# Performance work log

Measured on AMD Instinct MI355X. Metric: run time of the kernel, lower is better.

The kernel has to match this reference:

```python
import jax, jax.numpy as jnp
import numpy as np

N_NODES = 100000
N_EDGES = 1600000
IN_DIM, HID_DIM, OUT_DIM = 128, 128, 64


def _sage_conv(x, src, dst, W_l, W_r, b, num_nodes):
    # messages: gather source-node features, mean-aggregate at destination
    msgs = x[src]                                            # [E, D]
    agg = jax.ops.segment_sum(msgs, dst, num_segments=num_nodes)   # [N, D]
    deg = jax.ops.segment_sum(jnp.ones((src.shape[0],), x.dtype), dst,
                              num_segments=num_nodes)        # [N]
    mean = jnp.where(deg[:, None] > 0, agg / jnp.maximum(deg, 1.0)[:, None], 0.0)
    # PyG SAGEConv: lin_l(aggr) + lin_r(root); bias lives in lin_l
    return mean @ W_l + b + x @ W_r


def setup_inputs() -> dict:
    key = jax.random.key(0)
    ks = jax.random.split(key, 8)
    x = jax.random.normal(ks[0], (N_NODES, IN_DIM), dtype=jnp.float32)
    edge_index = jax.random.randint(ks[1], (2, N_EDGES), 0, N_NODES, dtype=jnp.int64)
    s1 = 1.0 / np.sqrt(IN_DIM)
    s2 = 1.0 / np.sqrt(HID_DIM)
    return {
        "x": x,
        "edge_index": edge_index,
        "W1_l": jax.random.normal(ks[2], (IN_DIM, HID_DIM), jnp.float32) * s1,
        "W1_r": jax.random.normal(ks[3], (IN_DIM, HID_DIM), jnp.float32) * s1,
        "b1": jnp.zeros((HID_DIM,), jnp.float32),
        "W2_l": jax.random.normal(ks[4], (HID_DIM, OUT_DIM), jnp.float32) * s2,
        "W2_r": jax.random.normal(ks[5], (HID_DIM, OUT_DIM), jnp.float32) * s2,
        "b2": jnp.zeros((OUT_DIM,), jnp.float32),
    }


def reference(x, edge_index, W1_l, W1_r, b1, W2_l, W2_r, b2):
    src, dst = edge_index[0], edge_index[1]  # source_to_target flow
    h = _sage_conv(x, src, dst, W1_l, W1_r, b1, N_NODES)
    h = jax.nn.relu(h)
    # dropout is identity in eval mode
    h = _sage_conv(h, src, dst, W2_l, W2_r, b2, N_NODES)
    return h
```

## Files before the change

### kernel.cpp

```cpp
#include <hip/hip_runtime.h>

#define N_NODES 100000
#define N_EDGES 1600000
#define IN_DIM 128
#define HID_DIM 128
#define OUT_DIM 64

#define BKT_SHIFT 8
#define NPB 256
#define NBKT ((N_NODES + NPB - 1) / NPB)
#define BKT_CAP 5120
#define BIN_CHUNK 4096

#define CC_CSR NBKT
#define CC_CONV (N_NODES / 4)
#define CC_WT 192

typedef __attribute__((ext_vector_type(8))) short short8;
typedef __attribute__((ext_vector_type(4))) float f32x4;
typedef __attribute__((ext_vector_type(2))) short s16x2;

__device__ __forceinline__ float bf2f(unsigned short h) {
    unsigned int u = ((unsigned int)h) << 16;
    return __builtin_bit_cast(float, u);
}
__device__ __forceinline__ unsigned short f2bf(float f) {
    unsigned int u = __builtin_bit_cast(unsigned int, f);
    u += 0x7FFFu + ((u >> 16) & 1u);
    return (unsigned short)(u >> 16);
}

#define XSCALE 21.166666f
#define XINV   0.047244094f
#define ZQ     10.583333f
#define ZINV   0.094488189f

__device__ __forceinline__ void acc_i8x4(unsigned v, s16x2& L, s16x2& H) {
    s16x2 sv = __builtin_bit_cast(s16x2, v);
    H += sv >> 8;
    L += (s16x2)(sv << 8) >> 8;
}

__device__ __forceinline__ int wswz(int m, int k, int KW) {
    return (m * KW + k) ^ ((m & 7) << 3);
}

__global__ __launch_bounds__(256) void bin_kernel(
        const int* __restrict__ src, const int* __restrict__ dst,
        int* __restrict__ cursor, unsigned* __restrict__ binned) {
    __shared__ int cnt[NBKT];
    __shared__ int sbase[NBKT];
    const int b = blockIdx.x, t = threadIdx.x;
    for (int i = t; i < NBKT; i += 256) cnt[i] = 0;
    __syncthreads();
    const int e0 = b * BIN_CHUNK;
    unsigned val[16];
    int bkt[16], rank[16];
    #pragma unroll
    for (int k = 0; k < 16; ++k) {
        int e = e0 + k * 256 + t;
        if (e < N_EDGES) {
            int d = dst[e];
            bkt[k] = d >> BKT_SHIFT;
            val[k] = (unsigned)src[e] | ((unsigned)(d & (NPB - 1)) << 17);
            rank[k] = atomicAdd(&cnt[bkt[k]], 1);
        } else {
            bkt[k] = -1;
        }
    }
    __syncthreads();
    for (int i = t; i < NBKT; i += 256)
        sbase[i] = cnt[i] ? atomicAdd(&cursor[i], cnt[i]) : 0;
    __syncthreads();
    #pragma unroll
    for (int k = 0; k < 16; ++k)
        if (bkt[k] >= 0)
            binned[(size_t)bkt[k] * BKT_CAP + sbase[bkt[k]] + rank[k]] = val[k];
}

__global__ __launch_bounds__(256) void csr_conv_kernel(
        const unsigned* __restrict__ binned, const int* __restrict__ cursor,
        int* __restrict__ offsets, int* __restrict__ csr_src,
        const float* __restrict__ x, unsigned short* __restrict__ xh,
        unsigned char* __restrict__ xq,
        const float* __restrict__ W1l, const float* __restrict__ W1r,
        const float* __restrict__ W2l, const float* __restrict__ W2r,
        unsigned short* __restrict__ WT1, unsigned short* __restrict__ WT2T) {
    int b = blockIdx.x;
    const int t = threadIdx.x;

    if (b < CC_CSR) {
        __shared__ int deg[NPB];
        __shared__ int cur[NPB];
        __shared__ int wsums[4];
        __shared__ int sbase_sh;
        const int lane = t & 63, wid = t >> 6;

        int ps = 0;
        for (int i = t; i < b; i += 256) ps += cursor[i];
        #pragma unroll
        for (int off = 32; off; off >>= 1) ps += __shfl_down(ps, off, 64);
        if (lane == 0) wsums[wid] = ps;
        deg[t] = 0;
        __syncthreads();
        if (t == 0) sbase_sh = wsums[0] + wsums[1] + wsums[2] + wsums[3];
        __syncthreads();
        const int base = sbase_sh;
        const int n0 = b << BKT_SHIFT;
        const int cnt = cursor[b];
        const unsigned* __restrict__ ebase = binned + (size_t)b * BKT_CAP;

        for (int i = t; i < cnt; i += 256)
            atomicAdd(&deg[ebase[i] >> 17], 1);
        __syncthreads();

        int d = deg[t];
        int s = d;
        #pragma unroll
        for (int off = 1; off < 64; off <<= 1) {
            int u = __shfl_up(s, off, 64);
            if (lane >= off) s += u;
        }
        if (lane == 63) wsums[wid] = s;
        __syncthreads();
        int add = 0;
        for (int w = 0; w < wid; ++w) add += wsums[w];
        const int excl = s + add - d;
        cur[t] = excl;
        const int n = n0 + t;
        if (n <= N_NODES) offsets[n] = base + excl;
        __syncthreads();

        for (int i = t; i < cnt; i += 256) {
            unsigned v = ebase[i];
            int pos = atomicAdd(&cur[v >> 17], 1);
            csr_src[base + pos] = (int)(v & 0x1FFFFu);
        }
        return;
    }

    b -= CC_CSR;
    if (b < CC_CONV) {
        const int w = t >> 6, lane = t & 63;
        const int row = b * 4 + w;
        float2 v = *(const float2*)(x + (size_t)row * 128 + lane * 2);
        unsigned pk = (unsigned)f2bf(v.x) | ((unsigned)f2bf(v.y) << 16);
        *(unsigned*)(xh + (size_t)row * 128 + lane * 2) = pk;
        int q0 = (int)__float2int_rn(fminf(fmaxf(v.x * XSCALE, -127.f), 127.f));
        int q1 = (int)__float2int_rn(fminf(fmaxf(v.y * XSCALE, -127.f), 127.f));
        *(unsigned short*)(xq + (size_t)row * 128 + lane * 2) =
            (unsigned short)((q0 & 0xFF) | ((q1 & 0xFF) << 8));
        return;
    }

    int i = (b - CC_CONV) * 256 + t;
    if (i < 128 * 256) {
        int m = i >> 8, k = i & 255;
        float v = (k < 128) ? W1l[(size_t)k * 128 + m] : W1r[(size_t)(k - 128) * 128 + m];
        WT1[wswz(m, k, 256)] = f2bf(v);
        return;
    }
    i -= 128 * 256;
    if (i < 128 * 128) {
        int j = i >> 7, k = i & 127;
        float v = (j < 64) ? W2l[(size_t)k * 64 + j] : W2r[(size_t)k * 64 + (j - 64)];
        WT2T[wswz(j, k, 128)] = f2bf(v);
    }
}

__global__ __launch_bounds__(256) void agg1_int8(
        const unsigned char* __restrict__ xq, const int* __restrict__ offsets,
        const int* __restrict__ csr_src, unsigned short* __restrict__ mh) {
    const int wv = threadIdx.x >> 6;
    const int lane = threadIdx.x & 63;
    const int slot = lane >> 3, dp = lane & 7;
    const int node = (blockIdx.x * 4 + wv) * 8 + slot;
    const int beg = offsets[node];
    const int deg = offsets[node + 1] - beg;

    s16x2 aL[4], aH[4];
    #pragma unroll
    for (int i = 0; i < 4; ++i) { aL[i] = (s16x2)0; aH[i] = (s16x2)0; }

    for (int c = 0; c < deg; c += 8) {
        int my = beg + c + dp;
        int idx8 = csr_src[my < beg + deg ? my : beg];
        #pragma unroll
        for (int jj = 0; jj < 8; ++jj) {
            if (c + jj < deg) {
                int s = __shfl(idx8, slot * 8 + jj, 64);
                uint4 v = *(const uint4*)(xq + (size_t)s * 128 + dp * 16);
                acc_i8x4(v.x, aL[0], aH[0]);
                acc_i8x4(v.y, aL[1], aH[1]);
                acc_i8x4(v.z, aL[2], aH[2]);
                acc_i8x4(v.w, aL[3], aH[3]);
            }
        }
    }

    const float inv = (deg > 0) ? XINV / (float)deg : 0.0f;
    unsigned w[8];
    #pragma unroll
    for (int d = 0; d < 4; ++d) {
        w[2 * d]     = (unsigned)f2bf((float)aL[d].x * inv)
                     | ((unsigned)f2bf((float)aH[d].x * inv) << 16);
        w[2 * d + 1] = (unsigned)f2bf((float)aL[d].y * inv)
                     | ((unsigned)f2bf((float)aH[d].y * inv) << 16);
    }
    uint4* o = (uint4*)(mh + (size_t)node * 128 + dp * 16);
    o[0] = make_uint4(w[0], w[1], w[2], w[3]);
    o[1] = make_uint4(w[4], w[5], w[6], w[7]);
}

__global__ __launch_bounds__(256) void gemm1_kernel(
        const unsigned short* __restrict__ mh, const unsigned short* __restrict__ xh,
        const unsigned short* __restrict__ WT1, const float* __restrict__ b1,
        unsigned short* __restrict__ hh) {
    __shared__ unsigned short Ws[128 * 256];
    const int t = threadIdx.x;
    {
        const uint4* s = (const uint4*)WT1;
        uint4* d = (uint4*)Ws;
        #pragma unroll
        for (int r = 0; r < 16; ++r) d[t + r * 256] = s[t + r * 256];
    }
    const int wave = t >> 6;
    const int lane = t & 63;
    const int rowbase = blockIdx.x * 128 + wave * 32;
    const int lrow = lane & 15;
    const int kq = (lane >> 4) * 8;
    const int rsw = (lrow & 7) << 3;

    f32x4 acc[2][8];
    #pragma unroll
    for (int rt = 0; rt < 2; ++rt)
        #pragma unroll
        for (int ct = 0; ct < 8; ++ct) acc[rt][ct] = (f32x4)0.f;

    int r0 = rowbase + lrow;      if (r0 > N_NODES - 1) r0 = N_NODES - 1;
    int r1 = rowbase + 16 + lrow; if (r1 > N_NODES - 1) r1 = N_NODES - 1;

    __syncthreads();

    #pragma unroll
    for (int half = 0; half < 2; ++half) {
        const unsigned short* __restrict__ A = half ? xh : mh;
        #pragma unroll
        for (int kc = 0; kc < 4; ++kc) {
            const int kofs = kc * 32 + kq;
            short8 a0 = *(const short8*)(A + (size_t)r0 * 128 + kofs);
            short8 a1 = *(const short8*)(A + (size_t)r1 * 128 + kofs);
            #pragma unroll
            for (int ct = 0; ct < 8; ++ct) {
                short8 bb = *(const short8*)&Ws[(((ct * 16 + lrow) << 8)
                                                 + (half << 7) + kofs) ^ rsw];
                acc[0][ct] = __builtin_amdgcn_mfma_f32_16x16x32_bf16(a0, bb, acc[0][ct], 0, 0, 0);
                acc[1][ct] = __builtin_amdgcn_mfma_f32_16x16x32_bf16(a1, bb, acc[1][ct], 0, 0, 0);
            }
        }
    }

    const int colq = lane & 15;
    const int rowq = (lane >> 4) * 4;
    #pragma unroll
    for (int ct = 0; ct < 8; ++ct) {
        const int col = ct * 16 + colq;
        const float bc = b1[col];
        #pragma unroll
        for (int rt = 0; rt < 2; ++rt) {
            #pragma unroll
            for (int i = 0; i < 4; ++i) {
                const int row = rowbase + rt * 16 + rowq + i;
                if (row < N_NODES)
                    hh[(size_t)row * 128 + col] = f2bf(fmaxf(acc[rt][ct][i] + bc, 0.f));
            }
        }
    }
}

__global__ __launch_bounds__(256) void gemm2_kernel(
        const unsigned short* __restrict__ hh, const unsigned short* __restrict__ WT2T,
        const float* __restrict__ b2, unsigned char* __restrict__ zq,
        unsigned short* __restrict__ pout) {
    __shared__ unsigned short Ws[128 * 128];
    const int t = threadIdx.x;
    {
        const uint4* s = (const uint4*)WT2T;
        uint4* d = (uint4*)Ws;
        #pragma unroll
        for (int r = 0; r < 8; ++r) d[t + r * 256] = s[t + r * 256];
    }
    const int wave = t >> 6;
    const int lane = t & 63;
    const int rowbase = blockIdx.x * 128 + wave * 32;
    const int lrow = lane & 15;
    const int kq = (lane >> 4) * 8;
    const int rsw = (lrow & 7) << 3;

    f32x4 acc[2][8];
    #pragma unroll
    for (int rt = 0; rt < 2; ++rt)
        #pragma unroll
        for (int ct = 0; ct < 8; ++ct) acc[rt][ct] = (f32x4)0.f;

    int r0 = rowbase + lrow;      if (r0 > N_NODES - 1) r0 = N_NODES - 1;
    int r1 = rowbase + 16 + lrow; if (r1 > N_NODES - 1) r1 = N_NODES - 1;

    __syncthreads();

    #pragma unroll
    for (int kc = 0; kc < 4; ++kc) {
        const int kofs = kc * 32 + kq;
        short8 a0 = *(const short8*)(hh + (size_t)r0 * 128 + kofs);
        short8 a1 = *(const short8*)(hh + (size_t)r1 * 128 + kofs);
        #pragma unroll
        for (int ct = 0; ct < 8; ++ct) {
            short8 bb = *(const short8*)&Ws[(((ct * 16 + lrow) << 7) + kofs) ^ rsw];
            acc[0][ct] = __builtin_amdgcn_mfma_f32_16x16x32_bf16(a0, bb, acc[0][ct], 0, 0, 0);
            acc[1][ct] = __builtin_amdgcn_mfma_f32_16x16x32_bf16(a1, bb, acc[1][ct], 0, 0, 0);
        }
    }

    const int colq = lane & 15;
    const int rowq = (lane >> 4) * 4;

    #pragma unroll
    for (int rt = 0; rt < 2; ++rt) {
        #pragma unroll
        for (int i = 0; i < 4; ++i) {
            const int row = rowbase + rt * 16 + rowq + i;
            if (row < N_NODES) {
                unsigned char* zr = zq + (size_t)row * 64 + colq;
                #pragma unroll
                for (int ct = 0; ct < 4; ++ct) {
                    float v = fminf(fmaxf(acc[rt][ct][i] * ZQ, -127.f), 127.f);
                    zr[ct * 16] = (unsigned char)(signed char)__float2int_rn(v);
                }
            }
        }
    }
    #pragma unroll
    for (int ct = 4; ct < 8; ++ct) {
        const int col = ct * 16 + colq;
        const float bc = b2[col - 64];
        #pragma unroll
        for (int rt = 0; rt < 2; ++rt) {
            #pragma unroll
            for (int i = 0; i < 4; ++i) {
                const int row = rowbase + rt * 16 + rowq + i;
                if (row < N_NODES)
                    pout[(size_t)row * 64 + (col - 64)] = f2bf(acc[rt][ct][i] + bc);
            }
        }
    }
}

__global__ __launch_bounds__(256) void agg2_out_kernel(
        const unsigned char* __restrict__ zq, const unsigned short* __restrict__ pout,
        const int* __restrict__ offsets, const int* __restrict__ csr_src,
        float* __restrict__ out) {
    const int wv = threadIdx.x >> 6;
    const int lane = threadIdx.x & 63;
    const int slot = lane >> 3, dp = lane & 7;
    const int node = (blockIdx.x * 4 + wv) * 8 + slot;
    const int beg = offsets[node];
    const int deg = offsets[node + 1] - beg;

    s16x2 aL[2], aH[2];
    #pragma unroll
    for (int i = 0; i < 2; ++i) { aL[i] = (s16x2)0; aH[i] = (s16x2)0; }

    for (int c = 0; c < deg; c += 8) {
        int my = beg + c + dp;
        int idx8 = csr_src[my < beg + deg ? my : beg];
        #pragma unroll
        for (int jj = 0; jj < 8; ++jj) {
            if (c + jj < deg) {
                int s = __shfl(idx8, slot * 8 + jj, 64);
                uint2 v = *(const uint2*)(zq + (size_t)s * 64 + dp * 8);
                acc_i8x4(v.x, aL[0], aH[0]);
                acc_i8x4(v.y, aL[1], aH[1]);
            }
        }
    }

    const float inv = (deg > 0) ? ZINV / (float)deg : 0.0f;
    const unsigned short* pp = pout + (size_t)node * 64 + dp * 8;
    float* oo = out + (size_t)node * 64 + dp * 8;
    #pragma unroll
    for (int d = 0; d < 2; ++d) {
        ushort4 p = *(const ushort4*)(pp + d * 4);
        float4 o;
        o.x = (float)aL[d].x * inv + bf2f(p.x);
        o.y = (float)aH[d].x * inv + bf2f(p.y);
        o.z = (float)aL[d].y * inv + bf2f(p.z);
        o.w = (float)aH[d].y * inv + bf2f(p.w);
        *(float4*)(oo + d * 4) = o;
    }
}


extern "C" void kernel_launch(void* const* d_in, const int* in_sizes, int n_in,
                              void* d_out, int out_size, void* d_ws, size_t ws_size,
                              hipStream_t stream) {
    const float* x   = (const float*)d_in[0];
    const int*   ei  = (const int*)d_in[1];
    const float* W1l = (const float*)d_in[2];
    const float* W1r = (const float*)d_in[3];
    const float* b1  = (const float*)d_in[4];
    const float* W2l = (const float*)d_in[5];
    const float* W2r = (const float*)d_in[6];
    const float* b2  = (const float*)d_in[7];
    float* out = (float*)d_out;

    const int* src = ei;
    const int* dst = ei + N_EDGES;

    char* ws = (char*)d_ws;
    int* cursor   = (int*)ws;
    int* offsets  = cursor + 512;
    int* csr_src  = offsets + N_NODES + 16;
    unsigned char*  xq  = (unsigned char*)(csr_src + N_EDGES + 64);
    unsigned short* xh  = (unsigned short*)(xq + (size_t)N_NODES * 128);
    unsigned short* mh  = xh + (size_t)N_NODES * 128;
    unsigned short* hh  = mh + (size_t)N_NODES * 128;
    unsigned char*  zq  = (unsigned char*)(hh + (size_t)N_NODES * 128);
    unsigned short* pout = (unsigned short*)(zq + (size_t)N_NODES * 64);
    unsigned short* WT1  = pout + (size_t)N_NODES * 64;
    unsigned short* WT2T = WT1 + 128 * 256;
    unsigned* binned = (unsigned*)mh;

    hipMemsetAsync(cursor, 0, NBKT * sizeof(int), stream);

    bin_kernel<<<(N_EDGES + BIN_CHUNK - 1) / BIN_CHUNK, 256, 0, stream>>>(
        src, dst, cursor, binned);

    csr_conv_kernel<<<CC_CSR + CC_CONV + CC_WT, 256, 0, stream>>>(
        binned, cursor, offsets, csr_src, x, xh, xq,
        W1l, W1r, W2l, W2r, WT1, WT2T);

    agg1_int8<<<N_NODES / 32, 256, 0, stream>>>(xq, offsets, csr_src, mh);
    gemm1_kernel<<<(N_NODES + 127) / 128, 256, 0, stream>>>(mh, xh, WT1, b1, hh);

    gemm2_kernel<<<(N_NODES + 127) / 128, 256, 0, stream>>>(hh, WT2T, b2, zq, pout);
    agg2_out_kernel<<<N_NODES / 32, 256, 0, stream>>>(zq, pout, offsets, csr_src, out);
}
```

Measured before the change: 193.5 us.

## Fuse layer-1 and layer-2 GEMMs, keeping hidden tile in LDS

```diff
diff --git a/kernel.cpp b/kernel.cpp
--- a/kernel.cpp
+++ b/kernel.cpp
@@ -212,17 +212,24 @@
     o[1] = make_uint4(w[4], w[5], w[6], w[7]);
 }
 
-__global__ __launch_bounds__(256) void gemm1_kernel(
+__global__ __launch_bounds__(256) void gemm12_kernel(
         const unsigned short* __restrict__ mh, const unsigned short* __restrict__ xh,
-        const unsigned short* __restrict__ WT1, const float* __restrict__ b1,
-        unsigned short* __restrict__ hh) {
-    __shared__ unsigned short Ws[128 * 256];
+        const unsigned short* __restrict__ WT1, const unsigned short* __restrict__ WT2T,
+        const float* __restrict__ b1, const float* __restrict__ b2,
+        unsigned char* __restrict__ zq, unsigned short* __restrict__ pout) {
+    __shared__ unsigned short Ws1[128 * 256];
+    __shared__ unsigned short Ws2[128 * 128];
+    __shared__ unsigned short hT[128][136];
     const int t = threadIdx.x;
     {
-        const uint4* s = (const uint4*)WT1;
-        uint4* d = (uint4*)Ws;
-        #pragma unroll
-        for (int r = 0; r < 16; ++r) d[t + r * 256] = s[t + r * 256];
+        const uint4* s1 = (const uint4*)WT1;
+        uint4* d1 = (uint4*)Ws1;
+        #pragma unroll
+        for (int r = 0; r < 16; ++r) d1[t + r * 256] = s1[t + r * 256];
+        const uint4* s2 = (const uint4*)WT2T;
+        uint4* d2 = (uint4*)Ws2;
+        #pragma unroll
+        for (int r = 0; r < 8; ++r) d2[t + r * 256] = s2[t + r * 256];
     }
     const int wave = t >> 6;
     const int lane = t & 63;
@@ -230,6 +237,8 @@
     const int lrow = lane & 15;
     const int kq = (lane >> 4) * 8;
     const int rsw = (lrow & 7) << 3;
+    const int colq = lane & 15;
+    const int rowq = (lane >> 4) * 4;
 
     f32x4 acc[2][8];
     #pragma unroll
@@ -252,16 +261,14 @@
             short8 a1 = *(const short8*)(A + (size_t)r1 * 128 + kofs);
             #pragma unroll
             for (int ct = 0; ct < 8; ++ct) {
-                short8 bb = *(const short8*)&Ws[(((ct * 16 + lrow) << 8)
-                                                 + (half << 7) + kofs) ^ rsw];
+                short8 bb = *(const short8*)&Ws1[(((ct * 16 + lrow) << 8)
+                                                  + (half << 7) + kofs) ^ rsw];
                 acc[0][ct] = __builtin_amdgcn_mfma_f32_16x16x32_bf16(a0, bb, acc[0][ct], 0, 0, 0);
                 acc[1][ct] = __builtin_amdgcn_mfma_f32_16x16x32_bf16(a1, bb, acc[1][ct], 0, 0, 0);
             }
         }
     }
 
-    const int colq = lane & 15;
-    const int rowq = (lane >> 4) * 4;
     #pragma unroll
     for (int ct = 0; ct < 8; ++ct) {
         const int col = ct * 16 + colq;
@@ -270,59 +277,29 @@
         for (int rt = 0; rt < 2; ++rt) {
             #pragma unroll
             for (int i = 0; i < 4; ++i) {
-                const int row = rowbase + rt * 16 + rowq + i;
-                if (row < N_NODES)
-                    hh[(size_t)row * 128 + col] = f2bf(fmaxf(acc[rt][ct][i] + bc, 0.f));
-            }
-        }
-    }
-}
-
-__global__ __launch_bounds__(256) void gemm2_kernel(
-        const unsigned short* __restrict__ hh, const unsigned short* __restrict__ WT2T,
-        const float* __restrict__ b2, unsigned char* __restrict__ zq,
-        unsigned short* __restrict__ pout) {
-    __shared__ unsigned short Ws[128 * 128];
-    const int t = threadIdx.x;
-    {
-        const uint4* s = (const uint4*)WT2T;
-        uint4* d = (uint4*)Ws;
-        #pragma unroll
-        for (int r = 0; r < 8; ++r) d[t + r * 256] = s[t + r * 256];
-    }
-    const int wave = t >> 6;
-    const int lane = t & 63;
-    const int rowbase = blockIdx.x * 128 + wave * 32;
-    const int lrow = lane & 15;
-    const int kq = (lane >> 4) * 8;
-    const int rsw = (lrow & 7) << 3;
-
-    f32x4 acc[2][8];
+                const int rl = wave * 32 + rt * 16 + rowq + i;
+                hT[rl][col] = f2bf(fmaxf(acc[rt][ct][i] + bc, 0.f));
+            }
+        }
+    }
+
     #pragma unroll
     for (int rt = 0; rt < 2; ++rt)
         #pragma unroll
         for (int ct = 0; ct < 8; ++ct) acc[rt][ct] = (f32x4)0.f;
-
-    int r0 = rowbase + lrow;      if (r0 > N_NODES - 1) r0 = N_NODES - 1;
-    int r1 = rowbase + 16 + lrow; if (r1 > N_NODES - 1) r1 = N_NODES - 1;
-
-    __syncthreads();
 
     #pragma unroll
     for (int kc = 0; kc < 4; ++kc) {
         const int kofs = kc * 32 + kq;
-        short8 a0 = *(const short8*)(hh + (size_t)r0 * 128 + kofs);
-        short8 a1 = *(const short8*)(hh + (size_t)r1 * 128 + kofs);
+        short8 a0 = *(const short8*)&hT[wave * 32 + lrow][kofs];
+        short8 a1 = *(const short8*)&hT[wave * 32 + 16 + lrow][kofs];
         #pragma unroll
         for (int ct = 0; ct < 8; ++ct) {
-            short8 bb = *(const short8*)&Ws[(((ct * 16 + lrow) << 7) + kofs) ^ rsw];
+            short8 bb = *(const short8*)&Ws2[(((ct * 16 + lrow) << 7) + kofs) ^ rsw];
             acc[0][ct] = __builtin_amdgcn_mfma_f32_16x16x32_bf16(a0, bb, acc[0][ct], 0, 0, 0);
             acc[1][ct] = __builtin_amdgcn_mfma_f32_16x16x32_bf16(a1, bb, acc[1][ct], 0, 0, 0);
         }
     }
-
-    const int colq = lane & 15;
-    const int rowq = (lane >> 4) * 4;
 
     #pragma unroll
     for (int rt = 0; rt < 2; ++rt) {
@@ -423,8 +400,7 @@
     unsigned char*  xq  = (unsigned char*)(csr_src + N_EDGES + 64);
     unsigned short* xh  = (unsigned short*)(xq + (size_t)N_NODES * 128);
     unsigned short* mh  = xh + (size_t)N_NODES * 128;
-    unsigned short* hh  = mh + (size_t)N_NODES * 128;
-    unsigned char*  zq  = (unsigned char*)(hh + (size_t)N_NODES * 128);
+    unsigned char*  zq  = (unsigned char*)(mh + (size_t)N_NODES * 128);
     unsigned short* pout = (unsigned short*)(zq + (size_t)N_NODES * 64);
     unsigned short* WT1  = pout + (size_t)N_NODES * 64;
     unsigned short* WT2T = WT1 + 128 * 256;
@@ -440,8 +416,9 @@
         W1l, W1r, W2l, W2r, WT1, WT2T);
 
     agg1_int8<<<N_NODES / 32, 256, 0, stream>>>(xq, offsets, csr_src, mh);
-    gemm1_kernel<<<(N_NODES + 127) / 128, 256, 0, stream>>>(mh, xh, WT1, b1, hh);
-
-    gemm2_kernel<<<(N_NODES + 127) / 128, 256, 0, stream>>>(hh, WT2T, b2, zq, pout);
+
+    gemm12_kernel<<<(N_NODES + 127) / 128, 256, 0, stream>>>(
+        mh, xh, WT1, WT2T, b1, b2, zq, pout);
+
     agg2_out_kernel<<<N_NODES / 32, 256, 0, stream>>>(zq, pout, offsets, csr_src, out);
 }
```

Measured after the change: 186.9 us. -3.4%, faster.
